# Optimization experiments

Hardware: AMD Instinct MI355X
Metric: run time of the kernel (lower is better)

Reference implementation:

```python
import jax, jax.numpy as jnp
import numpy as np
from jax import lax

B = 2048


def setup_inputs() -> dict:
    key = jax.random.key(0)
    ks = jax.random.split(key, 12)
    r = lambda k, s, sc=0.05: jax.random.normal(k, s, jnp.float32) * sc
    return {
        "w": jax.random.normal(ks[0], (B, 512), jnp.float32),
        "init_const": r(ks[1], (1, 512, 4, 4), 0.1),
        "init_conv_w": r(ks[2], (256, 512, 3, 3)),
        "init_conv_b": r(ks[3], (256,)),
        "aff1_w": r(ks[4], (256, 512)),
        "aff1_b": r(ks[5], (256,)),
        "conv1_w": r(ks[6], (128, 256, 3, 3)),
        "conv1_b": r(ks[7], (128,)),
        "aff2_w": r(ks[8], (128, 512)),
        "aff2_b": r(ks[9], (128,)),
        "conv2_w": r(ks[10], (64, 128, 3, 3)),
        "conv2_b": r(ks[11], (64,)),
    }


def _conv3(x, W):
    # 3x3 conv, stride 1, padding 1, NCHW / OIHW
    return lax.conv_general_dilated(x, W, (1, 1), ((1, 1), (1, 1)),
                                    dimension_numbers=("NCHW", "OIHW", "NCHW"))


def _lrelu(x):
    return jnp.where(x >= 0, x, 0.2 * x)


def reference(w, init_const, init_conv_w, init_conv_b,
              aff1_w, aff1_b, conv1_w, conv1_b,
              aff2_w, aff2_b, conv2_w, conv2_b):
    batch = w.shape[0]
    x = _conv3(init_const, init_conv_w) + init_conv_b[None, :, None, None]
    x = _lrelu(x)                                   # [1,256,4,4]
    x = jnp.broadcast_to(x, (batch,) + x.shape[1:])  # repeat over batch
    layers = ((aff1_w, aff1_b, conv1_w, conv1_b),
              (aff2_w, aff2_b, conv2_w, conv2_b))
    for aw, ab, cw, cb in layers:
        b_, c, h, wd = x.shape
        # bilinear upsample x2 (half-pixel centers == torch align_corners=False)
        x = jax.image.resize(x, (b_, c, 2 * h, 2 * wd), "bilinear")
        style = w @ aw.T + ab                        # [B, Cin]
        # modulated conv: conv(s*x, W) * demod, where
        # demod[b,o] = rsqrt(sum_{c,k} (s[b,c] W[o,c,k])^2 + 1e-8)
        xm = x * style[:, :, None, None]
        y = _conv3(xm, cw)                           # [B, Cout, 2h, 2w]
        w2 = jnp.sum(cw * cw, axis=(2, 3))           # [Cout, Cin]
        demod = lax.rsqrt(jnp.einsum("bc,oc->bo", style * style, w2) + 1e-8)
        x = _lrelu(y * demod[:, :, None, None] + cb[None, :, None, None])
    return x
```

## Files before the change

### kernel.cpp

```cpp
#include <hip/hip_runtime.h>
#include <hip/hip_fp16.h>

typedef _Float16 f16x8 __attribute__((ext_vector_type(8)));
typedef float f32x4 __attribute__((ext_vector_type(4)));

#define WS_X0U   0
#define WS_GHP   65536
#define WS_W2P   4259840
#define WS_WH    4407296
#define WS_AFTH  6504448
#define WS_W2TH  6897664
#define WS_S1P   7045120
#define WS_S2H   8093696
#define WS_SSQ   8617984
#define WS_D1    10190848
#define WS_D2    11239424
#define WS_X1T   11763712

__device__ __forceinline__ void up_wi(int j, int S, int& i0, int& i1,
                                      float& w0, float& w1) {
  int m = j >> 1;
  if (j & 1) { i0 = m; i1 = (m + 1 < S) ? m + 1 : S - 1; w0 = 0.75f; w1 = 0.25f; }
  else       { i0 = (m - 1 >= 0) ? m - 1 : 0; i1 = m;     w0 = 0.25f; w1 = 0.75f; }
}

__device__ __forceinline__ int xq_off(int pix, int i) {
  return (pix >> 1) * 64 + (((((pix & 1) << 2) + i) ^ ((pix >> 1) & 7)) << 3);
}

__global__ __launch_bounds__(256) void k_pre0(const float* __restrict__ ic,
    const float* __restrict__ w0c, const float* __restrict__ b0,
    const float* __restrict__ w1c, const float* __restrict__ w2c,
    const float* __restrict__ a1w, const float* __restrict__ a2w,
    const float* __restrict__ wsrc,
    float* __restrict__ x0u, _Float16* __restrict__ w2p,
    _Float16* __restrict__ wh, _Float16* __restrict__ afTh,
    _Float16* __restrict__ W2Th) {
  __shared__ float xl[512 * 16];
  __shared__ float part[16 * 257];
  __shared__ float part2[16 * 17];
  __shared__ float x4[16];
  int t = threadIdx.x;
  if (blockIdx.x < 256) {
    int o = blockIdx.x;
    for (int i = t; i < 512 * 16; i += 256) xl[i] = ic[i];
    __syncthreads();
    float acc[16];
#pragma unroll
    for (int p = 0; p < 16; ++p) acc[p] = 0.f;
#pragma unroll
    for (int it = 0; it < 18; ++it) {
      int j = it * 256 + t;
      float wv = w0c[o * 4608 + j];
      int c = j / 9, k = j - c * 9;
      int dy = k / 3, dx = k - dy * 3;
      const float* xc = &xl[c * 16];
#pragma unroll
      for (int p = 0; p < 16; ++p) {
        int py = p >> 2, px = p & 3;
        int iy = py + dy - 1, ix = px + dx - 1;
        bool ok = ((unsigned)iy < 4u) && ((unsigned)ix < 4u);
        float xv = ok ? xc[iy * 4 + ix] : 0.f;
        acc[p] += wv * xv;
      }
    }
#pragma unroll
    for (int p = 0; p < 16; ++p) part[p * 257 + t] = acc[p];
    __syncthreads();
    {
      int p = t & 15, ch = t >> 4;
      float s = 0.f;
#pragma unroll
      for (int g = 0; g < 16; ++g) s += part[p * 257 + ch * 16 + g];
      part2[p * 17 + ch] = s;
    }
    __syncthreads();
    if (t < 16) {
      float s = b0[o];
#pragma unroll
      for (int g = 0; g < 16; ++g) s += part2[t * 17 + g];
      x4[t] = (s >= 0.f) ? s : 0.2f * s;
    }
    __syncthreads();
    if (t < 64) {
      int oy = t >> 3, ox = t & 7;
      int y0, y1, xx0, xx1; float wy0, wy1, wx0, wx1;
      up_wi(oy, 4, y0, y1, wy0, wy1);
      up_wi(ox, 4, xx0, xx1, wx0, wx1);
      float v = wy0 * (wx0 * x4[y0 * 4 + xx0] + wx1 * x4[y0 * 4 + xx1])
              + wy1 * (wx0 * x4[y1 * 4 + xx0] + wx1 * x4[y1 * 4 + xx1]);
      x0u[o * 64 + t] = v;
    }
  } else {
    int idx = (blockIdx.x - 256) * 256 + t;
    if (idx < 73728) {
      int tap = idx / 8192, r = idx & 8191;
      int kg = r >> 11, mf = (r >> 9) & 3, l = (r >> 3) & 63, j = r & 7;
      int o = mf * 16 + (l & 15);
      int c = kg * 32 + (l >> 4) * 8 + j;
      w2p[idx] = (_Float16)w2c[(o * 128 + c) * 9 + tap];
    } else if (idx < 73728 + 1048576) {
      int i = idx - 73728;
      wh[i] = (_Float16)wsrc[i];
    } else if (idx < 73728 + 1048576 + 196608) {
      int i = idx - 73728 - 1048576;
      afTh[i] = (_Float16)((i < 131072) ? a1w[i] : a2w[i - 131072]);
    } else if (idx < 73728 + 1048576 + 196608 + 73728) {
      int i = idx - 73728 - 1048576 - 196608;
      int o = i / 384, k = i - o * 384;
      float v = 0.f;
      const float* wp = nullptr;
      if (o < 128 && k < 256)        wp = w1c + (o * 256 + k) * 9;
      else if (o >= 128 && k >= 256) wp = w2c + ((o - 128) * 128 + (k - 256)) * 9;
      if (wp) {
#pragma unroll
        for (int q = 0; q < 9; ++q) v += wp[q] * wp[q];
      }
      W2Th[i] = (_Float16)v;
    }
  }
}

__global__ __launch_bounds__(256) void k_pre1(const float* __restrict__ w1c,
    const float* __restrict__ x0u, _Float16* __restrict__ Ghp,
    const _Float16* __restrict__ wh, const _Float16* __restrict__ afTh,
    const float* __restrict__ a1b, const float* __restrict__ a2b,
    _Float16* __restrict__ s1p, _Float16* __restrict__ s2h,
    _Float16* __restrict__ ssq) {
  __shared__ _Float16 x0l[256][66];
  int t = threadIdx.x;
  if (blockIdx.x < 512) {
    int o = blockIdx.x >> 2, pg = blockIdx.x & 3;
    for (int i = t; i < 256 * 64; i += 256) {
      int c = i >> 6, p = i & 63;
      x0l[c][p] = (_Float16)x0u[i];
    }
    __syncthreads();
    int c = t;
    float wr9[9];
#pragma unroll
    for (int k = 0; k < 9; ++k) wr9[k] = w1c[(o * 256 + c) * 9 + k];
    int cpart = ((((c >> 3) & 3) * 16 + (o & 15)) * 8) + (c & 7);
    int cq = c >> 5, oq = o >> 4;
    for (int p = pg * 16; p < pg * 16 + 16; ++p) {
      int py = p >> 3, px = p & 7;
      float acc = 0.f;
#pragma unroll
      for (int dy = 0; dy < 3; ++dy) {
        int iy = py + dy - 1;
        if ((unsigned)iy >= 8u) continue;
#pragma unroll
        for (int dx = 0; dx < 3; ++dx) {
          int ix = px + dx - 1;
          if ((unsigned)ix >= 8u) continue;
          acc += wr9[dy * 3 + dx] * (float)x0l[c][iy * 8 + ix];
        }
      }
      Ghp[((p * 8 + oq) * 8 + cq) * 512 + cpart] = (_Float16)acc;
    }
  } else {
    int i = blockIdx.x - 512;
    int sx = i % 6, sy = i / 6;
    int lane = t & 63, w = t >> 6;
    int wr = w >> 1, wc = w & 1;
    int b0 = sy * 64 + wr * 32;
    int f0 = sx * 64 + wc * 32;
    f32x4 acc[2][2] = {};
    int lr = lane & 15, lk = (lane >> 4) * 8;
#pragma unroll
    for (int kg = 0; kg < 16; ++kg) {
      f16x8 af[2], bf[2];
#pragma unroll
      for (int mf = 0; mf < 2; ++mf)
        af[mf] = *(const f16x8*)(wh + (b0 + mf * 16 + lr) * 512 + kg * 32 + lk);
#pragma unroll
      for (int nf = 0; nf < 2; ++nf)
        bf[nf] = *(const f16x8*)(afTh + (f0 + nf * 16 + lr) * 512 + kg * 32 + lk);
#pragma unroll
      for (int mf = 0; mf < 2; ++mf)
#pragma unroll
        for (int nf = 0; nf < 2; ++nf)
          acc[mf][nf] = __builtin_amdgcn_mfma_f32_16x16x32_f16(af[mf], bf[nf], acc[mf][nf], 0, 0, 0);
    }
    int r4 = lane >> 4;
#pragma unroll
    for (int nf = 0; nf < 2; ++nf) {
      int f = f0 + nf * 16 + lr;
      float bias = (f < 256) ? a1b[f] : a2b[f - 256];
#pragma unroll
      for (int mf = 0; mf < 2; ++mf) {
#pragma unroll
        for (int r = 0; r < 4; ++r) {
          int b = b0 + mf * 16 + r4 * 4 + r;
          float v = acc[mf][nf][r] + bias;
          ssq[b * 384 + f] = (_Float16)(v * v);
          if (f < 256) {
            int flat = (((b >> 4) * 8 + (f >> 5)) * 64 + ((f >> 3) & 3) * 16 + (b & 15)) * 8 + (f & 7);
            s1p[flat] = (_Float16)v;
          } else {
            s2h[b * 128 + (f - 256)] = (_Float16)v;
          }
        }
      }
    }
  }
}

__global__ __launch_bounds__(256) void k_dmd(const _Float16* __restrict__ ssq,
    const _Float16* __restrict__ W2Th, float* __restrict__ d1,
    float* __restrict__ d2) {
  int t = threadIdx.x, lane = t & 63, w = t >> 6;
  int wr = w >> 1, wc = w & 1;
  int b0 = blockIdx.y * 64 + wr * 32;
  int o0 = blockIdx.x * 64 + wc * 32;
  int kbeg = (blockIdx.x == 2) ? 8 : 0;
  int kend = (blockIdx.x == 2) ? 12 : 8;
  f32x4 acc[2][2] = {};
  int lr = lane & 15, lk = (lane >> 4) * 8;
  for (int kg = kbeg; kg < kend; ++kg) {
    f16x8 af[2], bf[2];
#pragma unroll
    for (int mf = 0; mf < 2; ++mf)
      af[mf] = *(const f16x8*)(ssq + (b0 + mf * 16 + lr) * 384 + kg * 32 + lk);
#pragma unroll
    for (int nf = 0; nf < 2; ++nf)
      bf[nf] = *(const f16x8*)(W2Th + (o0 + nf * 16 + lr) * 384 + kg * 32 + lk);
#pragma unroll
    for (int mf = 0; mf < 2; ++mf)
#pragma unroll
      for (int nf = 0; nf < 2; ++nf)
        acc[mf][nf] = __builtin_amdgcn_mfma_f32_16x16x32_f16(af[mf], bf[nf], acc[mf][nf], 0, 0, 0);
  }
  int r4 = lane >> 4;
#pragma unroll
  for (int mf = 0; mf < 2; ++mf) {
#pragma unroll
    for (int r = 0; r < 4; ++r) {
      int b = b0 + mf * 16 + r4 * 4 + r;
#pragma unroll
      for (int nf = 0; nf < 2; ++nf) {
        int o = o0 + nf * 16 + lr;
        float v = rsqrtf(acc[mf][nf][r] + 1e-8f);
        if (o < 128) d1[b * 128 + o] = v;
        else         d2[b * 64 + (o - 128)] = v;
      }
    }
  }
}

__global__ __launch_bounds__(256) void k_l1(const _Float16* __restrict__ s1p,
    const _Float16* __restrict__ Ghp, const float* __restrict__ d1,
    const float* __restrict__ c1b, const _Float16* __restrict__ s2h,
    __half* __restrict__ x1t) {
  int t = threadIdx.x, lane = t & 63, w = t >> 6;
  int wr = w >> 1, wc = w & 1;
  int bq0 = blockIdx.y * 8 + wr * 4;
  int nq0 = blockIdx.x * 8 + wc * 4;
  f32x4 acc[4][4] = {};
#pragma unroll
  for (int kg = 0; kg < 8; ++kg) {
    f16x8 af[4], bf[4];
#pragma unroll
    for (int mf = 0; mf < 4; ++mf)
      af[mf] = *(const f16x8*)(s1p + (((bq0 + mf) * 8 + kg) * 64 + lane) * 8);
#pragma unroll
    for (int nf = 0; nf < 4; ++nf)
      bf[nf] = *(const f16x8*)(Ghp + (((nq0 + nf) * 8 + kg) * 64 + lane) * 8);
#pragma unroll
    for (int mf = 0; mf < 4; ++mf)
#pragma unroll
      for (int nf = 0; nf < 4; ++nf)
        acc[mf][nf] = __builtin_amdgcn_mfma_f32_16x16x32_f16(af[mf], bf[nf], acc[mf][nf], 0, 0, 0);
  }
  int nc = lane & 15, r4 = lane >> 4;
#pragma unroll
  for (int mf = 0; mf < 4; ++mf) {
#pragma unroll
    for (int r = 0; r < 4; ++r) {
      int b = (bq0 + mf) * 16 + r4 * 4 + r;
#pragma unroll
      for (int nf = 0; nf < 4; ++nf) {
        int n = (nq0 + nf) * 16 + nc;
        int o = n & 127, p = n >> 7;
        float v = acc[mf][nf][r] * d1[b * 128 + o] + c1b[o];
        v = (v >= 0.f) ? v : 0.2f * v;
        v *= (float)s2h[b * 128 + o];
        x1t[(b * 64 + p) * 128 + o] = (__half)v;
      }
    }
  }
}

__global__ __launch_bounds__(256, 2) void k_l2(const __half* __restrict__ x1t,
    const float* __restrict__ d2g, const _Float16* __restrict__ w2p,
    const float* __restrict__ c2b, float* __restrict__ out) {
  int b = blockIdx.x, t = threadIdx.x;
  int lane = t & 63, w = t >> 6;
  __shared__ unsigned short xq[2][9792];
  __shared__ unsigned short x1l[64 * 128];
  const __half* xb = x1t + b * 8192;

  for (int idx = t; idx < 1024; idx += 256) {
    int q = idx >> 4, gc = idx & 15;
    f16x8 v = *(const f16x8*)(xb + q * 128 + gc * 8);
    int gs = (gc & 8) | ((gc ^ q) & 7);
    *(f16x8*)&x1l[q * 128 + gs * 8] = v;
  }
  {
    f16x8 z = {};
    for (int idx = t; idx < 400; idx += 256) {
      int pg = idx >> 3, g = idx & 7;
      int buf = g >> 2, i = g & 3;
      int pix;
      if (pg < 18) pix = 288 + pg;
      else { int j = pg - 18; pix = (j >> 1) * 18 + (j & 1) * 17; }
      *(f16x8*)&xq[buf][xq_off(pix, i)] = z;
    }
  }
  f16x8 afb[3][4];
#pragma unroll
  for (int mf = 0; mf < 4; ++mf) {
    afb[0][mf] = *(const f16x8*)(w2p + (((0 * 4 + 0) * 4 + mf) * 64 + lane) * 8);
    afb[1][mf] = *(const f16x8*)(w2p + (((3 * 4 + 0) * 4 + mf) * 64 + lane) * 8);
  }
  int fy = t >> 4, fx = t & 15;
  int y0, y1, x0, x1i; float wy0, wy1, wx0, wx1;
  up_wi(fy, 8, y0, y1, wy0, wy1);
  up_wi(fx, 8, x0, x1i, wx0, wx1);
  _Float16 wA = (_Float16)(wy0 * wx0), wB = (_Float16)(wy0 * wx1);
  _Float16 wC = (_Float16)(wy1 * wx0), wD = (_Float16)(wy1 * wx1);
  int pixb = fy * 18 + fx + 1;
  int q00 = y0 * 8 + x0, q01 = y0 * 8 + x1i, q10 = y1 * 8 + x0, q11 = y1 * 8 + x1i;

  auto build_granule = [&](int qn, int i) {
    int gc = qn * 4 + i;
    f16x8 va = *(const f16x8*)&x1l[q00 * 128 + ((gc & 8) | ((gc ^ q00) & 7)) * 8];
    f16x8 vb = *(const f16x8*)&x1l[q01 * 128 + ((gc & 8) | ((gc ^ q01) & 7)) * 8];
    f16x8 vc = *(const f16x8*)&x1l[q10 * 128 + ((gc & 8) | ((gc ^ q10) & 7)) * 8];
    f16x8 vd = *(const f16x8*)&x1l[q11 * 128 + ((gc & 8) | ((gc ^ q11) & 7)) * 8];
    f16x8 v = va * wA;
    v += vb * wB;
    v += vc * wC;
    v += vd * wD;
    *(f16x8*)&xq[qn & 1][xq_off(pixb, i)] = v;
  };

  __syncthreads();
#pragma unroll
  for (int i = 0; i < 4; ++i) build_granule(0, i);
  __syncthreads();

  f32x4 acc[4][4] = {};
  f16x8 rw[2][6];
  int ig = lane >> 4;
  int colb = lane & 15;

  auto read_win = [&](int qb, int buf, int dx) {
#pragma unroll
    for (int j = 0; j < 6; ++j) {
      int fr = w * 4 + j - 1;
      int srow = ((unsigned)fr < 16u) ? fr : 16;
      int pix = srow * 18 + colb + dx;
      rw[buf][j] = *(const f16x8*)&xq[qb][xq_off(pix, ig)];
    }
  };

#pragma unroll
  for (int q = 0; q < 4; ++q) {
    read_win(q & 1, 0, 0);
#pragma unroll
    for (int dx = 0; dx < 3; ++dx) {
      if (dx < 2) read_win(q & 1, (dx + 1) & 1, dx + 1);
      if (q < 3) {
        if (dx == 0) { build_granule(q + 1, 0); build_granule(q + 1, 1); }
        else if (dx == 1) build_granule(q + 1, 2);
        else              build_granule(q + 1, 3);
      }
#pragma unroll
      for (int dy = 0; dy < 3; ++dy) {
        const int u = q * 9 + dx * 3 + dy;
        if (u + 2 < 36) {
          const int un = u + 2;
          const int qn = un / 9, rn = un - qn * 9;
          const int dxn = rn / 3, dyn = rn - dxn * 3;
          const int tapn = dyn * 3 + dxn;
#pragma unroll
          for (int mf = 0; mf < 4; ++mf)
            afb[un % 3][mf] = *(const f16x8*)(w2p + (((tapn * 4 + qn) * 4 + mf) * 64 + lane) * 8);
        }
        __builtin_amdgcn_s_setprio(1);
#pragma unroll
        for (int mf = 0; mf < 4; ++mf)
#pragma unroll
          for (int nf = 0; nf < 4; ++nf)
            acc[mf][nf] = __builtin_amdgcn_mfma_f32_16x16x32_f16(afb[u % 3][mf], rw[dx & 1][nf + dy], acc[mf][nf], 0, 0, 0);
        __builtin_amdgcn_s_setprio(0);
      }
    }
    if (q < 3) __syncthreads();
  }
  int px = lane & 15, r4 = lane >> 4;
#pragma unroll
  for (int mf = 0; mf < 4; ++mf) {
#pragma unroll
    for (int r = 0; r < 4; ++r) {
      int o = mf * 16 + r4 * 4 + r;
      float dm = d2g[b * 64 + o], bias = c2b[o];
#pragma unroll
      for (int nf = 0; nf < 4; ++nf) {
        int py = w * 4 + nf;
        float v = acc[mf][nf][r] * dm + bias;
        v = (v >= 0.f) ? v : 0.2f * v;
        out[(b * 64 + o) * 256 + py * 16 + px] = v;
      }
    }
  }
}

extern "C" void kernel_launch(void* const* d_in, const int* in_sizes, int n_in,
                              void* d_out, int out_size, void* d_ws, size_t ws_size,
                              hipStream_t stream) {
  const float* w    = (const float*)d_in[0];
  const float* ic   = (const float*)d_in[1];
  const float* w0c  = (const float*)d_in[2];
  const float* b0   = (const float*)d_in[3];
  const float* a1w  = (const float*)d_in[4];
  const float* a1b  = (const float*)d_in[5];
  const float* w1c  = (const float*)d_in[6];
  const float* c1b  = (const float*)d_in[7];
  const float* a2w  = (const float*)d_in[8];
  const float* a2b  = (const float*)d_in[9];
  const float* w2c  = (const float*)d_in[10];
  const float* c2b  = (const float*)d_in[11];
  float* out = (float*)d_out;
  char* ws = (char*)d_ws;

  float*    x0u  = (float*)(ws + WS_X0U);
  _Float16* Ghp  = (_Float16*)(ws + WS_GHP);
  _Float16* w2p  = (_Float16*)(ws + WS_W2P);
  _Float16* wh   = (_Float16*)(ws + WS_WH);
  _Float16* afTh = (_Float16*)(ws + WS_AFTH);
  _Float16* W2Th = (_Float16*)(ws + WS_W2TH);
  _Float16* s1p  = (_Float16*)(ws + WS_S1P);
  _Float16* s2h  = (_Float16*)(ws + WS_S2H);
  _Float16* ssq  = (_Float16*)(ws + WS_SSQ);
  float*    d1   = (float*)(ws + WS_D1);
  float*    d2   = (float*)(ws + WS_D2);
  __half*   x1t  = (__half*)(ws + WS_X1T);

  k_pre0 <<<5696, 256, 0, stream>>>(ic, w0c, b0, w1c, w2c, a1w, a2w, w,
                                    x0u, w2p, wh, afTh, W2Th);
  k_pre1 <<<704, 256, 0, stream>>>(w1c, x0u, Ghp, wh, afTh, a1b, a2b,
                                   s1p, s2h, ssq);
  dim3 gd(3, 32);
  k_dmd  <<<gd, 256, 0, stream>>>(ssq, W2Th, d1, d2);
  dim3 g1(64, 16);
  k_l1   <<<g1, 256, 0, stream>>>(s1p, Ghp, d1, c1b, s2h, x1t);
  k_l2   <<<2048, 256, 0, stream>>>(x1t, d2, w2p, c2b, out);
}
```

Baseline: 140.5 us.

## Split k_l2 output channels across two waves per row band with 512-thread blocks

Doubles the k_l2 block to 512 threads so that each row band is handled by two waves, each computing half of the 64 output channels. This halves the per-wave accumulator and A-fragment registers and shares the upsample granule build across the two thread halves. The double-buffered read window is dropped in favour of a single window reload per dx, which gives up some LDS/MFMA overlap in return for more waves per CU and lower register pressure.

```diff
diff --git a/kernel.cpp b/kernel.cpp
--- a/kernel.cpp
+++ b/kernel.cpp
@@ -291,16 +291,17 @@
   }
 }
 
-__global__ __launch_bounds__(256, 2) void k_l2(const __half* __restrict__ x1t,
+__global__ __launch_bounds__(512, 4) void k_l2(const __half* __restrict__ x1t,
     const float* __restrict__ d2g, const _Float16* __restrict__ w2p,
     const float* __restrict__ c2b, float* __restrict__ out) {
   int b = blockIdx.x, t = threadIdx.x;
   int lane = t & 63, w = t >> 6;
+  int wr = w >> 1, wo = w & 1;
   __shared__ unsigned short xq[2][9792];
   __shared__ unsigned short x1l[64 * 128];
   const __half* xb = x1t + b * 8192;
 
-  for (int idx = t; idx < 1024; idx += 256) {
+  for (int idx = t; idx < 1024; idx += 512) {
     int q = idx >> 4, gc = idx & 15;
     f16x8 v = *(const f16x8*)(xb + q * 128 + gc * 8);
     int gs = (gc & 8) | ((gc ^ q) & 7);
@@ -308,7 +309,7 @@
   }
   {
     f16x8 z = {};
-    for (int idx = t; idx < 400; idx += 256) {
+    for (int idx = t; idx < 400; idx += 512) {
       int pg = idx >> 3, g = idx & 7;
       int buf = g >> 2, i = g & 3;
       int pix;
@@ -317,13 +318,14 @@
       *(f16x8*)&xq[buf][xq_off(pix, i)] = z;
     }
   }
-  f16x8 afb[3][4];
-#pragma unroll
-  for (int mf = 0; mf < 4; ++mf) {
-    afb[0][mf] = *(const f16x8*)(w2p + (((0 * 4 + 0) * 4 + mf) * 64 + lane) * 8);
-    afb[1][mf] = *(const f16x8*)(w2p + (((3 * 4 + 0) * 4 + mf) * 64 + lane) * 8);
-  }
-  int fy = t >> 4, fx = t & 15;
+  f16x8 afb[3][2];
+#pragma unroll
+  for (int mf = 0; mf < 2; ++mf) {
+    afb[0][mf] = *(const f16x8*)(w2p + (((0 * 4 + 0) * 4 + wo * 2 + mf) * 64 + lane) * 8);
+    afb[1][mf] = *(const f16x8*)(w2p + (((3 * 4 + 0) * 4 + wo * 2 + mf) * 64 + lane) * 8);
+  }
+  int tp = t & 255, gp = t >> 8;
+  int fy = tp >> 4, fx = tp & 15;
   int y0, y1, x0, x1i; float wy0, wy1, wx0, wx1;
   up_wi(fy, 8, y0, y1, wy0, wy1);
   up_wi(fx, 8, x0, x1i, wx0, wx1);
@@ -346,36 +348,27 @@
   };
 
   __syncthreads();
-#pragma unroll
-  for (int i = 0; i < 4; ++i) build_granule(0, i);
+  build_granule(0, gp * 2);
+  build_granule(0, gp * 2 + 1);
   __syncthreads();
 
-  f32x4 acc[4][4] = {};
-  f16x8 rw[2][6];
+  f32x4 acc[2][4] = {};
+  f16x8 rw[6];
   int ig = lane >> 4;
   int colb = lane & 15;
 
-  auto read_win = [&](int qb, int buf, int dx) {
-#pragma unroll
-    for (int j = 0; j < 6; ++j) {
-      int fr = w * 4 + j - 1;
-      int srow = ((unsigned)fr < 16u) ? fr : 16;
-      int pix = srow * 18 + colb + dx;
-      rw[buf][j] = *(const f16x8*)&xq[qb][xq_off(pix, ig)];
-    }
-  };
-
 #pragma unroll
   for (int q = 0; q < 4; ++q) {
-    read_win(q & 1, 0, 0);
 #pragma unroll
     for (int dx = 0; dx < 3; ++dx) {
-      if (dx < 2) read_win(q & 1, (dx + 1) & 1, dx + 1);
-      if (q < 3) {
-        if (dx == 0) { build_granule(q + 1, 0); build_granule(q + 1, 1); }
-        else if (dx == 1) build_granule(q + 1, 2);
-        else              build_granule(q + 1, 3);
-      }
+#pragma unroll
+      for (int j = 0; j < 6; ++j) {
+        int fr = wr * 4 + j - 1;
+        int srow = ((unsigned)fr < 16u) ? fr : 16;
+        int pix = srow * 18 + colb + dx;
+        rw[j] = *(const f16x8*)&xq[q & 1][xq_off(pix, ig)];
+      }
+      if (q < 3 && dx < 2) build_granule(q + 1, gp * 2 + dx);
 #pragma unroll
       for (int dy = 0; dy < 3; ++dy) {
         const int u = q * 9 + dx * 3 + dy;
@@ -385,15 +378,15 @@
           const int dxn = rn / 3, dyn = rn - dxn * 3;
           const int tapn = dyn * 3 + dxn;
 #pragma unroll
-          for (int mf = 0; mf < 4; ++mf)
-            afb[un % 3][mf] = *(const f16x8*)(w2p + (((tapn * 4 + qn) * 4 + mf) * 64 + lane) * 8);
+          for (int mf = 0; mf < 2; ++mf)
+            afb[un % 3][mf] = *(const f16x8*)(w2p + (((tapn * 4 + qn) * 4 + wo * 2 + mf) * 64 + lane) * 8);
         }
         __builtin_amdgcn_s_setprio(1);
 #pragma unroll
-        for (int mf = 0; mf < 4; ++mf)
+        for (int mf = 0; mf < 2; ++mf)
 #pragma unroll
           for (int nf = 0; nf < 4; ++nf)
-            acc[mf][nf] = __builtin_amdgcn_mfma_f32_16x16x32_f16(afb[u % 3][mf], rw[dx & 1][nf + dy], acc[mf][nf], 0, 0, 0);
+            acc[mf][nf] = __builtin_amdgcn_mfma_f32_16x16x32_f16(afb[u % 3][mf], rw[nf + dy], acc[mf][nf], 0, 0, 0);
         __builtin_amdgcn_s_setprio(0);
       }
     }
@@ -401,14 +394,14 @@
   }
   int px = lane & 15, r4 = lane >> 4;
 #pragma unroll
-  for (int mf = 0; mf < 4; ++mf) {
+  for (int mf = 0; mf < 2; ++mf) {
 #pragma unroll
     for (int r = 0; r < 4; ++r) {
-      int o = mf * 16 + r4 * 4 + r;
+      int o = (wo * 2 + mf) * 16 + r4 * 4 + r;
       float dm = d2g[b * 64 + o], bias = c2b[o];
 #pragma unroll
       for (int nf = 0; nf < 4; ++nf) {
-        int py = w * 4 + nf;
+        int py = wr * 4 + nf;
         float v = acc[mf][nf][r] * dm + bias;
         v = (v >= 0.f) ? v : 0.2f * v;
         out[(b * 64 + o) * 256 + py * 16 + px] = v;
@@ -456,5 +449,5 @@
   k_dmd  <<<gd, 256, 0, stream>>>(ssq, W2Th, d1, d2);
   dim3 g1(64, 16);
   k_l1   <<<g1, 256, 0, stream>>>(s1p, Ghp, d1, c1b, s2h, x1t);
-  k_l2   <<<2048, 256, 0, stream>>>(x1t, d2, w2p, c2b, out);
-}
+  k_l2   <<<2048, 512, 0, stream>>>(x1t, d2, w2p, c2b, out);
+}
```

Result: slower. 152.5 us (+8.6%).
